# Performance work log

Measured on AMD Instinct MI355X. Metric: run time of the kernel, lower is better.

Reference implementation:

```python
import jax, jax.numpy as jnp
import numpy as np

N_NODES = 100000
N_EDGES = 600000
IN_CH = 128
HID = 128


def setup_inputs() -> dict:
    key = jax.random.key(0)
    ks = jax.random.split(key, 8)
    x = jax.random.normal(ks[0], (N_NODES, IN_CH), dtype=jnp.float32)
    edge_index = jax.random.randint(ks[1], (2, N_EDGES), 0, N_NODES, dtype=jnp.int64)
    # Linear weights stored as (in, out); scaled like torch default init
    W1 = jax.random.normal(ks[2], (2 * IN_CH, HID), dtype=jnp.float32) / np.sqrt(2 * IN_CH)
    b1 = jnp.zeros((HID,), dtype=jnp.float32)
    W2 = jax.random.normal(ks[3], (HID, HID), dtype=jnp.float32) / np.sqrt(HID)
    b2 = jnp.zeros((HID,), dtype=jnp.float32)
    W3 = jax.random.normal(ks[4], (HID, 1), dtype=jnp.float32) / np.sqrt(HID)
    b3 = jnp.zeros((1,), dtype=jnp.float32)
    return {"x": x, "edge_index": edge_index, "W1": W1, "b1": b1,
            "W2": W2, "b2": b2, "W3": W3, "b3": b3}


def reference(x, edge_index, W1, b1, W2, b2, W3, b3):
    src = edge_index[0]
    tgt = edge_index[1]
    # gather + concat: [n_edges, 2*in_channels]
    h = jnp.concatenate([x[src, :], x[tgt, :]], axis=1)
    h = jax.nn.elu(h @ W1 + b1)
    h = jax.nn.elu(h @ W2 + b2)
    h = h @ W3 + b3  # [n_edges, 1]
    return jnp.squeeze(h)  # squeeze=True path -> [n_edges]
```

## Files before the change

kernel.cpp:

```cpp
#include <hip/hip_runtime.h>

#define N_NODES 100000
#define N_EDGES 600000
#define NT2 9375
#define LDW 264
#define LDH 136
typedef _Float16 f16x8 __attribute__((ext_vector_type(8)));
typedef __attribute__((ext_vector_type(4))) float f32x4;

__device__ __forceinline__ float elu_f(float v) {
    return v > 0.0f ? v : (__expf(v) - 1.0f);
}

extern "C" __global__ __launch_bounds__(256)
void k0_convert(const float* __restrict__ x, const float* __restrict__ W1,
                _Float16* __restrict__ xh, _Float16* __restrict__ W1f) {
    const int t = threadIdx.x;
    if (blockIdx.x < 16) {
        const int id = blockIdx.x * 256 + t;
        const int lane = id & 63, f = id >> 6;
        const int ks = f & 3, c = (f >> 2) & 1, half = (f >> 3) & 1, w = f >> 4;
        const int ln = lane & 15, kg = lane >> 4;
        const int col = w * 32 + c * 16 + ln;
        f16x8 v;
#pragma unroll
        for (int j = 0; j < 8; ++j)
            v[j] = (_Float16)W1[(half * 128 + ks * 32 + kg * 8 + j) * 128 + col];
        *(f16x8*)(W1f + (size_t)id * 8) = v;
    }
    const int step = gridDim.x * blockDim.x;
    for (int c = blockIdx.x * blockDim.x + t; c < (N_NODES * 128) / 8; c += step) {
        const float4 a0 = *(const float4*)(x + (size_t)c * 8);
        const float4 a1 = *(const float4*)(x + (size_t)c * 8 + 4);
        f16x8 h;
        h[0] = (_Float16)a0.x; h[1] = (_Float16)a0.y;
        h[2] = (_Float16)a0.z; h[3] = (_Float16)a0.w;
        h[4] = (_Float16)a1.x; h[5] = (_Float16)a1.y;
        h[6] = (_Float16)a1.z; h[7] = (_Float16)a1.w;
        *(f16x8*)(xh + (size_t)c * 8) = h;
    }
}

extern "C" __global__ __launch_bounds__(256, 3)
void k2_edge_mlp(const _Float16* __restrict__ xh, const void* __restrict__ eiv,
                 const _Float16* __restrict__ W1f, const float* __restrict__ b1,
                 const float* __restrict__ W2, const float* __restrict__ b2,
                 const float* __restrict__ W3, const float* __restrict__ b3,
                 float* __restrict__ out) {
    __shared__ __align__(16) _Float16 sRaw[64 * LDW];
    __shared__ __align__(16) _Float16 sH1[64 * LDH];
    __shared__ float sPart[4][64];
    __shared__ int sFlag;

    const int t = threadIdx.x;
    const int w = t >> 6, lane = t & 63;
    const int ln = lane & 15, kg = lane >> 4;
    const int row_s = t >> 2;
    const int qb = (t & 3) * 32;
    const float b3v = b3[0];
    const int stride = gridDim.x;

    if (t < 64) {
        unsigned v = ((const unsigned*)eiv)[2 * t + 1];
        unsigned long long bm = __ballot(v == 0u);
        if (t == 0) sFlag = (bm == ~0ull) ? 1 : 0;
    }

    const _Float16* w1w = W1f + (size_t)(w * 16) * 512;

    f16x8 bf2[2][4];
#pragma unroll
    for (int c = 0; c < 2; ++c) {
        const int n = w * 32 + c * 16 + ln;
#pragma unroll
        for (int ks = 0; ks < 4; ++ks) {
            f16x8 v;
#pragma unroll
            for (int j = 0; j < 8; ++j) {
                int k = ks * 32 + kg * 8 + j;
                v[j] = (_Float16)W2[k * 128 + n];
            }
            bf2[c][ks] = v;
        }
    }

    float b1v[2], b2v[2], w3v[2];
#pragma unroll
    for (int c = 0; c < 2; ++c) {
        int col = w * 32 + c * 16 + ln;
        b1v[c] = b1[col]; b2v[c] = b2[col]; w3v[c] = W3[col];
    }

    __syncthreads();
    const int mode64 = sFlag;
    const int tile0 = blockIdx.x;

    int se_nx, ge_nx;
    {
        int e = tile0 * 64 + row_s;
        int se, ge;
        if (mode64) {
            se = (int)((const long long*)eiv)[e];
            ge = (int)((const long long*)eiv)[N_EDGES + e];
        } else {
            se = ((const int*)eiv)[e];
            ge = ((const int*)eiv)[N_EDGES + e];
        }
        const _Float16* pa = xh + (size_t)se * 128 + qb;
        const _Float16* pb = xh + (size_t)ge * 128 + qb;
#pragma unroll
        for (int i = 0; i < 4; ++i) {
            f16x8 ga = *(const f16x8*)(pa + i * 8);
            f16x8 gb = *(const f16x8*)(pb + i * 8);
            *(f16x8*)(&sRaw[row_s * LDW + qb + i * 8]) = ga;
            *(f16x8*)(&sRaw[row_s * LDW + 128 + qb + i * 8]) = gb;
        }
    }
    {
        int t1 = tile0 + stride;
        int t1c = (t1 < NT2) ? t1 : tile0;
        int e = t1c * 64 + row_s;
        if (mode64) {
            se_nx = (int)((const long long*)eiv)[e];
            ge_nx = (int)((const long long*)eiv)[N_EDGES + e];
        } else {
            se_nx = ((const int*)eiv)[e];
            ge_nx = ((const int*)eiv)[N_EDGES + e];
        }
    }
    __syncthreads();

    int prevE0 = -1;
    for (int tile = tile0; tile < NT2; tile += stride) {
        const int nt = tile + stride;
        const int ntc = (nt < NT2) ? nt : tile;

        const _Float16* pa = xh + (size_t)se_nx * 128 + qb;
        const _Float16* pb = xh + (size_t)ge_nx * 128 + qb;
        f16x8 Ga[4], Gb[4];
#pragma unroll
        for (int i = 0; i < 4; ++i) {
            Ga[i] = *(const f16x8*)(pa + i * 8);
            Gb[i] = *(const f16x8*)(pb + i * 8);
        }

        {
            int n2 = nt + stride;
            int n2c = (n2 < NT2) ? n2 : ntc;
            int e = n2c * 64 + row_s;
            if (mode64) {
                se_nx = (int)((const long long*)eiv)[e];
                ge_nx = (int)((const long long*)eiv)[N_EDGES + e];
            } else {
                se_nx = ((const int*)eiv)[e];
                ge_nx = ((const int*)eiv)[N_EDGES + e];
            }
        }

        f32x4 acc1[4][2];
#pragma unroll
        for (int rt = 0; rt < 4; ++rt)
#pragma unroll
            for (int c = 0; c < 2; ++c) acc1[rt][c] = (f32x4){0.f, 0.f, 0.f, 0.f};

#pragma unroll 1
        for (int ks = 0; ks < 4; ++ks) {
            f16x8 w1f[2][2];
#pragma unroll
            for (int half = 0; half < 2; ++half)
#pragma unroll
                for (int c = 0; c < 2; ++c)
                    w1f[half][c] = *(const f16x8*)(
                        w1w + ((half * 8 + c * 4 + ks) * 64 + lane) * 8);
#pragma unroll
            for (int rt = 0; rt < 4; ++rt) {
                f16x8 a_s = *(const f16x8*)(&sRaw[(rt * 16 + ln) * LDW + ks * 32 + kg * 8]);
                f16x8 a_t = *(const f16x8*)(&sRaw[(rt * 16 + ln) * LDW + 128 + ks * 32 + kg * 8]);
#pragma unroll
                for (int c = 0; c < 2; ++c) {
                    acc1[rt][c] = __builtin_amdgcn_mfma_f32_16x16x32_f16(
                        a_s, w1f[0][c], acc1[rt][c], 0, 0, 0);
                    acc1[rt][c] = __builtin_amdgcn_mfma_f32_16x16x32_f16(
                        a_t, w1f[1][c], acc1[rt][c], 0, 0, 0);
                }
            }
        }
        __syncthreads();

        if (prevE0 >= 0 && t < 64)
            out[prevE0 + t] = sPart[0][t] + sPart[1][t] +
                              sPart[2][t] + sPart[3][t] + b3v;

#pragma unroll
        for (int rt = 0; rt < 4; ++rt)
#pragma unroll
            for (int c = 0; c < 2; ++c) {
                const int col = w * 32 + c * 16 + ln;
#pragma unroll
                for (int reg = 0; reg < 4; ++reg) {
                    const int row = rt * 16 + kg * 4 + reg;
                    sH1[row * LDH + col] =
                        (_Float16)elu_f(acc1[rt][c][reg] + b1v[c]);
                }
            }

#pragma unroll
        for (int i = 0; i < 4; ++i) {
            *(f16x8*)(&sRaw[row_s * LDW + qb + i * 8]) = Ga[i];
            *(f16x8*)(&sRaw[row_s * LDW + 128 + qb + i * 8]) = Gb[i];
        }
        __syncthreads();

        f32x4 acc2[4][2];
#pragma unroll
        for (int rt = 0; rt < 4; ++rt)
#pragma unroll
            for (int c = 0; c < 2; ++c) acc2[rt][c] = (f32x4){0.f, 0.f, 0.f, 0.f};

#pragma unroll
        for (int ks = 0; ks < 4; ++ks) {
#pragma unroll
            for (int rt = 0; rt < 4; ++rt) {
                f16x8 a = *(const f16x8*)(&sH1[(rt * 16 + ln) * LDH + ks * 32 + kg * 8]);
#pragma unroll
                for (int c = 0; c < 2; ++c)
                    acc2[rt][c] = __builtin_amdgcn_mfma_f32_16x16x32_f16(
                        a, bf2[c][ks], acc2[rt][c], 0, 0, 0);
            }
        }

#pragma unroll
        for (int rt = 0; rt < 4; ++rt) {
            float pr[4] = {0.f, 0.f, 0.f, 0.f};
#pragma unroll
            for (int c = 0; c < 2; ++c) {
#pragma unroll
                for (int reg = 0; reg < 4; ++reg)
                    pr[reg] += elu_f(acc2[rt][c][reg] + b2v[c]) * w3v[c];
            }
#pragma unroll
            for (int m = 1; m < 16; m <<= 1)
#pragma unroll
                for (int reg = 0; reg < 4; ++reg) pr[reg] += __shfl_xor(pr[reg], m, 64);
            if (ln == 0) {
#pragma unroll
                for (int reg = 0; reg < 4; ++reg)
                    sPart[w][rt * 16 + kg * 4 + reg] = pr[reg];
            }
        }

        prevE0 = tile * 64;
    }

    __syncthreads();
    if (prevE0 >= 0 && t < 64)
        out[prevE0 + t] = sPart[0][t] + sPart[1][t] +
                          sPart[2][t] + sPart[3][t] + b3v;
}

extern "C" void kernel_launch(void* const* d_in, const int* in_sizes, int n_in,
                              void* d_out, int out_size, void* d_ws, size_t ws_size,
                              hipStream_t stream) {
    const float* x  = (const float*)d_in[0];
    const void*  ei = d_in[1];
    const float* W1 = (const float*)d_in[2];
    const float* b1 = (const float*)d_in[3];
    const float* W2 = (const float*)d_in[4];
    const float* b2 = (const float*)d_in[5];
    const float* W3 = (const float*)d_in[6];
    const float* b3 = (const float*)d_in[7];
    float* out = (float*)d_out;

    _Float16* xh  = (_Float16*)((char*)d_ws + 256);
    _Float16* W1f = xh + (size_t)N_NODES * 128;

    k0_convert<<<2048, 256, 0, stream>>>(x, W1, xh, W1f);
    k2_edge_mlp<<<768, 256, 0, stream>>>(xh, ei, W1f, b1, W2, b2, W3, b3, out);
}
```

Measured before the change: 205.9 us.

## Split edge-MLP tile across 8 waves with 16 output columns each

```diff
diff --git a/kernel.cpp b/kernel.cpp
--- a/kernel.cpp
+++ b/kernel.cpp
@@ -19,9 +19,9 @@
     if (blockIdx.x < 16) {
         const int id = blockIdx.x * 256 + t;
         const int lane = id & 63, f = id >> 6;
-        const int ks = f & 3, c = (f >> 2) & 1, half = (f >> 3) & 1, w = f >> 4;
+        const int ks = f & 3, c = (f >> 2) & 1, half = (f >> 3) & 1, w4 = f >> 4;
         const int ln = lane & 15, kg = lane >> 4;
-        const int col = w * 32 + c * 16 + ln;
+        const int col = w4 * 32 + c * 16 + ln;
         f16x8 v;
 #pragma unroll
         for (int j = 0; j < 8; ++j)
@@ -41,7 +41,7 @@
     }
 }
 
-extern "C" __global__ __launch_bounds__(256, 3)
+extern "C" __global__ __launch_bounds__(512, 2)
 void k2_edge_mlp(const _Float16* __restrict__ xh, const void* __restrict__ eiv,
                  const _Float16* __restrict__ W1f, const float* __restrict__ b1,
                  const float* __restrict__ W2, const float* __restrict__ b2,
@@ -49,14 +49,14 @@
                  float* __restrict__ out) {
     __shared__ __align__(16) _Float16 sRaw[64 * LDW];
     __shared__ __align__(16) _Float16 sH1[64 * LDH];
-    __shared__ float sPart[4][64];
+    __shared__ float sPart[8][64];
     __shared__ int sFlag;
 
     const int t = threadIdx.x;
     const int w = t >> 6, lane = t & 63;
     const int ln = lane & 15, kg = lane >> 4;
-    const int row_s = t >> 2;
-    const int qb = (t & 3) * 32;
+    const int row_s = t >> 3;
+    const int qb = (t & 7) * 16;
     const float b3v = b3[0];
     const int stride = gridDim.x;
 
@@ -66,12 +66,11 @@
         if (t == 0) sFlag = (bm == ~0ull) ? 1 : 0;
     }
 
-    const _Float16* w1w = W1f + (size_t)(w * 16) * 512;
-
-    f16x8 bf2[2][4];
-#pragma unroll
-    for (int c = 0; c < 2; ++c) {
-        const int n = w * 32 + c * 16 + ln;
+    const _Float16* w1w = W1f + (size_t)((w >> 1) * 16 + (w & 1) * 4) * 512;
+
+    f16x8 bf2[4];
+    {
+        const int n = w * 16 + ln;
 #pragma unroll
         for (int ks = 0; ks < 4; ++ks) {
             f16x8 v;
@@ -80,16 +79,12 @@
                 int k = ks * 32 + kg * 8 + j;
                 v[j] = (_Float16)W2[k * 128 + n];
             }
-            bf2[c][ks] = v;
-        }
-    }
-
-    float b1v[2], b2v[2], w3v[2];
-#pragma unroll
-    for (int c = 0; c < 2; ++c) {
-        int col = w * 32 + c * 16 + ln;
-        b1v[c] = b1[col]; b2v[c] = b2[col]; w3v[c] = W3[col];
-    }
+            bf2[ks] = v;
+        }
+    }
+
+    const int coln = w * 16 + ln;
+    const float b1v = b1[coln], b2v = b2[coln], w3v = W3[coln];
 
     __syncthreads();
     const int mode64 = sFlag;
@@ -109,7 +104,7 @@
         const _Float16* pa = xh + (size_t)se * 128 + qb;
         const _Float16* pb = xh + (size_t)ge * 128 + qb;
 #pragma unroll
-        for (int i = 0; i < 4; ++i) {
+        for (int i = 0; i < 2; ++i) {
             f16x8 ga = *(const f16x8*)(pa + i * 8);
             f16x8 gb = *(const f16x8*)(pb + i * 8);
             *(f16x8*)(&sRaw[row_s * LDW + qb + i * 8]) = ga;
@@ -137,9 +132,9 @@
 
         const _Float16* pa = xh + (size_t)se_nx * 128 + qb;
         const _Float16* pb = xh + (size_t)ge_nx * 128 + qb;
-        f16x8 Ga[4], Gb[4];
-#pragma unroll
-        for (int i = 0; i < 4; ++i) {
+        f16x8 Ga[2], Gb[2];
+#pragma unroll
+        for (int i = 0; i < 2; ++i) {
             Ga[i] = *(const f16x8*)(pa + i * 8);
             Gb[i] = *(const f16x8*)(pb + i * 8);
         }
@@ -157,87 +152,71 @@
             }
         }
 
-        f32x4 acc1[4][2];
-#pragma unroll
-        for (int rt = 0; rt < 4; ++rt)
-#pragma unroll
-            for (int c = 0; c < 2; ++c) acc1[rt][c] = (f32x4){0.f, 0.f, 0.f, 0.f};
+        f32x4 acc1[4];
+#pragma unroll
+        for (int rt = 0; rt < 4; ++rt) acc1[rt] = (f32x4){0.f, 0.f, 0.f, 0.f};
 
 #pragma unroll 1
         for (int ks = 0; ks < 4; ++ks) {
-            f16x8 w1f[2][2];
+            f16x8 w1f[2];
 #pragma unroll
             for (int half = 0; half < 2; ++half)
-#pragma unroll
-                for (int c = 0; c < 2; ++c)
-                    w1f[half][c] = *(const f16x8*)(
-                        w1w + ((half * 8 + c * 4 + ks) * 64 + lane) * 8);
+                w1f[half] = *(const f16x8*)(
+                    w1w + ((half * 8 + ks) * 64 + lane) * 8);
 #pragma unroll
             for (int rt = 0; rt < 4; ++rt) {
                 f16x8 a_s = *(const f16x8*)(&sRaw[(rt * 16 + ln) * LDW + ks * 32 + kg * 8]);
                 f16x8 a_t = *(const f16x8*)(&sRaw[(rt * 16 + ln) * LDW + 128 + ks * 32 + kg * 8]);
-#pragma unroll
-                for (int c = 0; c < 2; ++c) {
-                    acc1[rt][c] = __builtin_amdgcn_mfma_f32_16x16x32_f16(
-                        a_s, w1f[0][c], acc1[rt][c], 0, 0, 0);
-                    acc1[rt][c] = __builtin_amdgcn_mfma_f32_16x16x32_f16(
-                        a_t, w1f[1][c], acc1[rt][c], 0, 0, 0);
-                }
+                acc1[rt] = __builtin_amdgcn_mfma_f32_16x16x32_f16(
+                    a_s, w1f[0], acc1[rt], 0, 0, 0);
+                acc1[rt] = __builtin_amdgcn_mfma_f32_16x16x32_f16(
+                    a_t, w1f[1], acc1[rt], 0, 0, 0);
             }
         }
         __syncthreads();
 
-        if (prevE0 >= 0 && t < 64)
-            out[prevE0 + t] = sPart[0][t] + sPart[1][t] +
-                              sPart[2][t] + sPart[3][t] + b3v;
+        if (prevE0 >= 0 && t < 64) {
+            float s = b3v;
+#pragma unroll
+            for (int ww = 0; ww < 8; ++ww) s += sPart[ww][t];
+            out[prevE0 + t] = s;
+        }
 
 #pragma unroll
         for (int rt = 0; rt < 4; ++rt)
 #pragma unroll
-            for (int c = 0; c < 2; ++c) {
-                const int col = w * 32 + c * 16 + ln;
-#pragma unroll
-                for (int reg = 0; reg < 4; ++reg) {
-                    const int row = rt * 16 + kg * 4 + reg;
-                    sH1[row * LDH + col] =
-                        (_Float16)elu_f(acc1[rt][c][reg] + b1v[c]);
-                }
-            }
-
-#pragma unroll
-        for (int i = 0; i < 4; ++i) {
+            for (int reg = 0; reg < 4; ++reg) {
+                const int row = rt * 16 + kg * 4 + reg;
+                sH1[row * LDH + coln] = (_Float16)elu_f(acc1[rt][reg] + b1v);
+            }
+
+#pragma unroll
+        for (int i = 0; i < 2; ++i) {
             *(f16x8*)(&sRaw[row_s * LDW + qb + i * 8]) = Ga[i];
             *(f16x8*)(&sRaw[row_s * LDW + 128 + qb + i * 8]) = Gb[i];
         }
         __syncthreads();
 
-        f32x4 acc2[4][2];
-#pragma unroll
-        for (int rt = 0; rt < 4; ++rt)
-#pragma unroll
-            for (int c = 0; c < 2; ++c) acc2[rt][c] = (f32x4){0.f, 0.f, 0.f, 0.f};
+        f32x4 acc2[4];
+#pragma unroll
+        for (int rt = 0; rt < 4; ++rt) acc2[rt] = (f32x4){0.f, 0.f, 0.f, 0.f};
 
 #pragma unroll
         for (int ks = 0; ks < 4; ++ks) {
 #pragma unroll
             for (int rt = 0; rt < 4; ++rt) {
                 f16x8 a = *(const f16x8*)(&sH1[(rt * 16 + ln) * LDH + ks * 32 + kg * 8]);
-#pragma unroll
-                for (int c = 0; c < 2; ++c)
-                    acc2[rt][c] = __builtin_amdgcn_mfma_f32_16x16x32_f16(
-                        a, bf2[c][ks], acc2[rt][c], 0, 0, 0);
+                acc2[rt] = __builtin_amdgcn_mfma_f32_16x16x32_f16(
+                    a, bf2[ks], acc2[rt], 0, 0, 0);
             }
         }
 
 #pragma unroll
         for (int rt = 0; rt < 4; ++rt) {
-            float pr[4] = {0.f, 0.f, 0.f, 0.f};
-#pragma unroll
-            for (int c = 0; c < 2; ++c) {
-#pragma unroll
-                for (int reg = 0; reg < 4; ++reg)
-                    pr[reg] += elu_f(acc2[rt][c][reg] + b2v[c]) * w3v[c];
-            }
+            float pr[4];
+#pragma unroll
+            for (int reg = 0; reg < 4; ++reg)
+                pr[reg] = elu_f(acc2[rt][reg] + b2v) * w3v;
 #pragma unroll
             for (int m = 1; m < 16; m <<= 1)
 #pragma unroll
@@ -253,9 +232,12 @@
     }
 
     __syncthreads();
-    if (prevE0 >= 0 && t < 64)
-        out[prevE0 + t] = sPart[0][t] + sPart[1][t] +
-                          sPart[2][t] + sPart[3][t] + b3v;
+    if (prevE0 >= 0 && t < 64) {
+        float s = b3v;
+#pragma unroll
+        for (int ww = 0; ww < 8; ++ww) s += sPart[ww][t];
+        out[prevE0 + t] = s;
+    }
 }
 
 extern "C" void kernel_launch(void* const* d_in, const int* in_sizes, int n_in,
@@ -275,5 +257,5 @@
     _Float16* W1f = xh + (size_t)N_NODES * 128;
 
     k0_convert<<<2048, 256, 0, stream>>>(x, W1, xh, W1f);
-    k2_edge_mlp<<<768, 256, 0, stream>>>(xh, ei, W1f, b1, W2, b2, W3, b3, out);
-}
+    k2_edge_mlp<<<512, 512, 0, stream>>>(xh, ei, W1f, b1, W2, b2, W3, b3, out);
+}
```

New measurement: 242.2 us. 17.7% more time.
